# Performance work log

Measured on AMD Instinct MI355X. Metric: run time of the kernel, lower is better.

## Reference

```python
import jax, jax.numpy as jnp
import numpy as np

N, L, S, H, D = 2, 4096, 4096, 8, 32


def setup_inputs() -> dict:
    key = jax.random.key(0)
    kq, kk, kv, km = jax.random.split(key, 4)
    queries = jax.random.normal(kq, (N, L, H, D), dtype=jnp.float32)
    keys = jax.random.normal(kk, (N, S, H, D), dtype=jnp.float32)
    values = jax.random.normal(kv, (N, S, H, D), dtype=jnp.float32)
    q_mask = jnp.ones((N, L), dtype=bool)
    kv_mask = jax.random.randint(km, (N, S), 0, 2).astype(bool)
    return {"queries": queries, "keys": keys, "values": values,
            "q_mask": q_mask, "kv_mask": kv_mask}


def reference(queries, keys, values, q_mask, kv_mask):
    # QK: [N, L, S, H] -- contraction over head dim D (GEMM form of the
    # original broadcast-multiply-sum).
    QK = jnp.einsum('nlhd,nshd->nlsh', queries, keys)
    mask = q_mask[:, :, None] & kv_mask[:, None, :]            # [N, L, S]
    QK = jnp.where(mask[..., None], QK, -jnp.inf)
    softmax_temp = 1.0 / np.sqrt(D).astype(np.float32)
    A = jax.nn.softmax(softmax_temp * QK, axis=2)              # softmax over S
    # weighted value sum: [N, L, H, D]
    return jnp.einsum('nlsh,nshd->nlhd', A, values)
```

## Files before the change

### kernel.cpp

```cpp
#include <hip/hip_runtime.h>
#include <stdint.h>
#include <math.h>


typedef __bf16 bf16x8 __attribute__((ext_vector_type(8)));
typedef float  f32x16 __attribute__((ext_vector_type(16)));
typedef float  f32x4  __attribute__((ext_vector_type(4)));

#define C2 0.25502407414058425f

#define BUF_OFF_B 64

__global__ __launch_bounds__(256) void prep(
    const float* __restrict__ K, const float* __restrict__ V,
    const int* __restrict__ KM, int* __restrict__ W, __bf16* __restrict__ BUF)
{
    const int wib = threadIdx.x >> 6, lane = threadIdx.x & 63;
    const int n = blockIdx.x >> 8;
    __shared__ int csum[64];
    __shared__ int idx[4096];

    const int* m = KM + n * 4096;
    for (int c = wib; c < 64; c += 4) {
        unsigned long long bal = __ballot(m[c * 64 + lane] != 0);
        if (lane == 0) csum[c] = __popcll(bal);
    }
    __syncthreads();
    if (wib == 0) {
        int v = csum[lane];
        #pragma unroll
        for (int off = 1; off < 64; off <<= 1) {
            int u = __shfl_up(v, off);
            if (lane >= off) v += u;
        }
        csum[lane] = v;
    }
    __syncthreads();
    const int total = csum[63];
    for (int c = wib; c < 64; c += 4) {
        bool mm = m[c * 64 + lane] != 0;
        unsigned long long bal = __ballot(mm);
        int base = c ? csum[c - 1] : 0;
        int pre = __popcll(bal & ((1ull << lane) - 1ull));
        if (mm) idx[base + pre] = c * 64 + lane;
    }
    const int cnt32 = (total + 31) & ~31;
    for (int j = total + (int)threadIdx.x; j < cnt32; j += 256) idx[j] = 0;
    __syncthreads();

    if (threadIdx.x == 0 && (blockIdx.x & 255) == 0) W[n] = total;

    const int gt = blockIdx.x * 4 + wib;
    const int h = (gt >> 7) & 7, t = gt & 127;
    if (t >= ((total + 31) >> 5)) return;
    const int hi = lane >> 5, lq = lane & 31;
    const float* Kb = K + (size_t)n * 4096 * 256 + h * 32;
    const float* Vb = V + (size_t)n * 4096 * 256 + h * 32;
    __bf16* dst = BUF + (size_t)gt * 2048 + lane * 8;

    const float* krow = Kb + (size_t)idx[t * 32 + lq] * 256 + 8 * hi;
    #pragma unroll
    for (int f = 0; f < 2; ++f) {
        f32x4 a = *(const f32x4*)(krow + 16 * f);
        f32x4 b = *(const f32x4*)(krow + 16 * f + 4);
        bf16x8 o8;
        o8[0] = (__bf16)a[0]; o8[1] = (__bf16)a[1]; o8[2] = (__bf16)a[2]; o8[3] = (__bf16)a[3];
        o8[4] = (__bf16)b[0]; o8[5] = (__bf16)b[1]; o8[6] = (__bf16)b[2]; o8[7] = (__bf16)b[3];
        *(bf16x8*)(dst + f * 512) = o8;
    }
    #pragma unroll
    for (int f = 0; f < 2; ++f) {
        bf16x8 o8;
        #pragma unroll
        for (int j = 0; j < 8; ++j) {
            int s = t * 32 + 16 * f + (j & 3) + 4 * hi + 8 * ((j >> 2) & 1);
            o8[j] = (__bf16)Vb[(size_t)idx[s] * 256 + lq];
        }
        *(bf16x8*)(dst + 1024 + f * 512) = o8;
    }
}

__global__ __launch_bounds__(256, 4) void fattn32(
    const float* __restrict__ Q, const __bf16* __restrict__ BUF,
    const int* __restrict__ W, float* __restrict__ Out)
{
    constexpr int L = 4096, H = 8, D = 32, RS = H * D;
    const int lane = threadIdx.x & 63;
    const int wib  = threadIdx.x >> 6;
    const int w    = (blockIdx.x & 7) * 256 + (blockIdx.x >> 3);
    const int qt   = w & 127;
    const int h    = (w >> 7) & 7;
    const int n    = w >> 10;
    const int hi   = lane >> 5;
    const int lq   = lane & 31;

    const int cnt    = W[n];
    const int ntiles = (cnt + 31) >> 5;

    const float* qrow = Q + ((size_t)n * L + qt * 32 + lq) * RS + h * D + 8 * hi;
    bf16x8 qf0, qf1;
    {
        f32x4 a0 = *(const f32x4*)(qrow);
        f32x4 b0 = *(const f32x4*)(qrow + 4);
        f32x4 a1 = *(const f32x4*)(qrow + 16);
        f32x4 b1 = *(const f32x4*)(qrow + 20);
        #pragma unroll
        for (int j = 0; j < 4; ++j) {
            qf0[j]     = (__bf16)(C2 * a0[j]);
            qf0[4 + j] = (__bf16)(C2 * b0[j]);
            qf1[j]     = (__bf16)(C2 * a1[j]);
            qf1[4 + j] = (__bf16)(C2 * b1[j]);
        }
    }

    const __bf16* bufp = BUF + (size_t)((n * 8 + h) * 128) * 2048 + lane * 8;

    f32x16 o = {};
    float l = 0.0f;
    const f32x16 z = {};

    int t = wib;
    const __bf16* tb = bufp + (size_t)t * 2048;
    bf16x8 ck0 = *(const bf16x8*)(tb);
    bf16x8 ck1 = *(const bf16x8*)(tb + 512);
    bf16x8 cv0 = *(const bf16x8*)(tb + 1024);
    bf16x8 cv1 = *(const bf16x8*)(tb + 1536);

    for (; t < ntiles; t += 4) {
        const int tn = (t + 4 < ntiles) ? t + 4 : t;
        const __bf16* nb = bufp + (size_t)tn * 2048;
        bf16x8 nk0 = *(const bf16x8*)(nb);
        bf16x8 nk1 = *(const bf16x8*)(nb + 512);
        bf16x8 nv0 = *(const bf16x8*)(nb + 1024);
        bf16x8 nv1 = *(const bf16x8*)(nb + 1536);

        f32x16 st = __builtin_amdgcn_mfma_f32_32x32x16_bf16(ck0, qf0, z, 0, 0, 0);
        st = __builtin_amdgcn_mfma_f32_32x32x16_bf16(ck1, qf1, st, 0, 0, 0);

        float p[16];
        #pragma unroll
        for (int r = 0; r < 16; ++r)
            p[r] = __builtin_amdgcn_exp2f(st[r]);

        const int kb = t * 32;
        if (kb + 32 > cnt) {
            #pragma unroll
            for (int r = 0; r < 16; ++r) {
                int ks = kb + (r & 3) + 8 * ((r >> 2) & 1) + 16 * (r >> 3) + 4 * hi;
                if (ks >= cnt) p[r] = 0.0f;
            }
        }

        l += (((p[0] + p[1]) + (p[2] + p[3])) + ((p[4] + p[5]) + (p[6] + p[7])))
           + (((p[8] + p[9]) + (p[10] + p[11])) + ((p[12] + p[13]) + (p[14] + p[15])));

        bf16x8 pf0, pf1;
        #pragma unroll
        for (int j = 0; j < 8; ++j) { pf0[j] = (__bf16)p[j]; pf1[j] = (__bf16)p[8 + j]; }

        o = __builtin_amdgcn_mfma_f32_32x32x16_bf16(cv0, pf0, o, 0, 0, 0);
        o = __builtin_amdgcn_mfma_f32_32x32x16_bf16(cv1, pf1, o, 0, 0, 0);

        ck0 = nk0; ck1 = nk1; cv0 = nv0; cv1 = nv1;
    }

    __shared__ float xt[4][32 * 33];
    __shared__ float Ls[4][32];

    float lt = l + __shfl_xor(l, 32);
    float* tp = xt[wib];
    #pragma unroll
    for (int r = 0; r < 16; ++r) {
        int d = (r & 3) + 8 * (r >> 2) + 4 * hi;
        tp[lq * 33 + d] = o[r];
    }
    if (hi == 0) Ls[wib][lq] = lt;
    __syncthreads();

    const int q  = threadIdx.x >> 3;
    const int dg = (threadIdx.x & 7) * 4;
    float ltot = Ls[0][q] + Ls[1][q] + Ls[2][q] + Ls[3][q];
    float inv = 1.0f / ltot;
    f32x4 acc = {};
    #pragma unroll
    for (int wv = 0; wv < 4; ++wv) {
        #pragma unroll
        for (int jj = 0; jj < 4; ++jj)
            acc[jj] += xt[wv][q * 33 + dg + jj];
    }
    acc[0] *= inv; acc[1] *= inv; acc[2] *= inv; acc[3] *= inv;
    float* orow = Out + (((size_t)(n * L + qt * 32 + q)) * H + h) * D + dg;
    *(f32x4*)orow = acc;
}

extern "C" void kernel_launch(void* const* d_in, const int* in_sizes, int n_in,
                              void* d_out, int out_size, void* d_ws, size_t ws_size,
                              hipStream_t stream) {
    const float* Q = (const float*)d_in[0];
    const float* K = (const float*)d_in[1];
    const float* V = (const float*)d_in[2];
    const int* KM = (const int*)d_in[4];
    float* Out = (float*)d_out;

    int* Wk = (int*)d_ws;
    __bf16* BUF = (__bf16*)((char*)d_ws + BUF_OFF_B);

    hipLaunchKernelGGL(prep,    dim3(512),  dim3(256), 0, stream, K, V, KM, Wk, BUF);
    hipLaunchKernelGGL(fattn32, dim3(2048), dim3(256), 0, stream, Q, BUF, Wk, Out);
}
```

Before: 45.09 us.

## Share K/V tiles across four query tiles per block via LDS double buffering

Each block now handles four query tiles of the same head, one per wave, instead of splitting the key range of a single query tile across waves. The K/V tile is staged cooperatively into LDS with a double buffer and a barrier each iteration, so each tile is fetched from global memory once per block rather than once per wave. This also drops the cross-wave reduction at the end, because each wave normalises and writes its own output. The cost is a barrier per key tile and 4x fewer blocks (512), which reduces parallelism and latency hiding.

```diff
diff --git a/kernel.cpp b/kernel.cpp
--- a/kernel.cpp
+++ b/kernel.cpp
@@ -84,20 +84,22 @@
     const float* __restrict__ Q, const __bf16* __restrict__ BUF,
     const int* __restrict__ W, float* __restrict__ Out)
 {
-    constexpr int L = 4096, H = 8, D = 32, RS = H * D;
-    const int lane = threadIdx.x & 63;
-    const int wib  = threadIdx.x >> 6;
-    const int w    = (blockIdx.x & 7) * 256 + (blockIdx.x >> 3);
-    const int qt   = w & 127;
-    const int h    = (w >> 7) & 7;
-    const int n    = w >> 10;
-    const int hi   = lane >> 5;
-    const int lq   = lane & 31;
+    const int tid  = threadIdx.x;
+    const int lane = tid & 63;
+    const int wib  = tid >> 6;
+    const int b  = blockIdx.x;
+    const int w  = (b & 7) * 64 + (b >> 3);
+    const int qg = w & 31;
+    const int h  = (w >> 5) & 7;
+    const int n  = w >> 8;
+    const int qt = qg * 4 + wib;
+    const int hi = lane >> 5;
+    const int lq = lane & 31;
 
     const int cnt    = W[n];
     const int ntiles = (cnt + 31) >> 5;
 
-    const float* qrow = Q + ((size_t)n * L + qt * 32 + lq) * RS + h * D + 8 * hi;
+    const float* qrow = Q + ((size_t)n * 4096 + qt * 32 + lq) * 256 + h * 32 + 8 * hi;
     bf16x8 qf0, qf1;
     {
         f32x4 a0 = *(const f32x4*)(qrow);
@@ -113,29 +115,32 @@
         }
     }
 
-    const __bf16* bufp = BUF + (size_t)((n * 8 + h) * 128) * 2048 + lane * 8;
+    __shared__ float pool[4352];
+    uint8_t* sb = (uint8_t*)pool;
+
+    const uint8_t* bufbase = (const uint8_t*)BUF + (size_t)((n * 8 + h) * 128) * 4096;
+    const uint8_t* ssrc = bufbase + tid * 16;
 
     f32x16 o = {};
     float l = 0.0f;
     const f32x16 z = {};
 
-    int t = wib;
-    const __bf16* tb = bufp + (size_t)t * 2048;
-    bf16x8 ck0 = *(const bf16x8*)(tb);
-    bf16x8 ck1 = *(const bf16x8*)(tb + 512);
-    bf16x8 cv0 = *(const bf16x8*)(tb + 1024);
-    bf16x8 cv1 = *(const bf16x8*)(tb + 1536);
-
-    for (; t < ntiles; t += 4) {
-        const int tn = (t + 4 < ntiles) ? t + 4 : t;
-        const __bf16* nb = bufp + (size_t)tn * 2048;
-        bf16x8 nk0 = *(const bf16x8*)(nb);
-        bf16x8 nk1 = *(const bf16x8*)(nb + 512);
-        bf16x8 nv0 = *(const bf16x8*)(nb + 1024);
-        bf16x8 nv1 = *(const bf16x8*)(nb + 1536);
-
-        f32x16 st = __builtin_amdgcn_mfma_f32_32x32x16_bf16(ck0, qf0, z, 0, 0, 0);
-        st = __builtin_amdgcn_mfma_f32_32x32x16_bf16(ck1, qf1, st, 0, 0, 0);
+    uint4 stg = *(const uint4*)(ssrc);
+
+    for (int t = 0; t < ntiles; ++t) {
+        *(uint4*)(sb + (t & 1) * 4096 + tid * 16) = stg;
+        if (t + 1 < ntiles)
+            stg = *(const uint4*)(ssrc + (size_t)(t + 1) * 4096);
+        asm volatile("s_waitcnt lgkmcnt(0)\n\ts_barrier" ::: "memory");
+
+        const __bf16* tb = (const __bf16*)(sb + (t & 1) * 4096) + lane * 8;
+        bf16x8 kf0 = *(const bf16x8*)(tb);
+        bf16x8 kf1 = *(const bf16x8*)(tb + 512);
+        bf16x8 vf0 = *(const bf16x8*)(tb + 1024);
+        bf16x8 vf1 = *(const bf16x8*)(tb + 1536);
+
+        f32x16 st = __builtin_amdgcn_mfma_f32_32x32x16_bf16(kf0, qf0, z, 0, 0, 0);
+        st = __builtin_amdgcn_mfma_f32_32x32x16_bf16(kf1, qf1, st, 0, 0, 0);
 
         float p[16];
         #pragma unroll
@@ -158,39 +163,33 @@
         #pragma unroll
         for (int j = 0; j < 8; ++j) { pf0[j] = (__bf16)p[j]; pf1[j] = (__bf16)p[8 + j]; }
 
-        o = __builtin_amdgcn_mfma_f32_32x32x16_bf16(cv0, pf0, o, 0, 0, 0);
-        o = __builtin_amdgcn_mfma_f32_32x32x16_bf16(cv1, pf1, o, 0, 0, 0);
-
-        ck0 = nk0; ck1 = nk1; cv0 = nv0; cv1 = nv1;
-    }
-
-    __shared__ float xt[4][32 * 33];
-    __shared__ float Ls[4][32];
-
-    float lt = l + __shfl_xor(l, 32);
-    float* tp = xt[wib];
+        o = __builtin_amdgcn_mfma_f32_32x32x16_bf16(vf0, pf0, o, 0, 0, 0);
+        o = __builtin_amdgcn_mfma_f32_32x32x16_bf16(vf1, pf1, o, 0, 0, 0);
+    }
+
+    float lt  = l + __shfl_xor(l, 32);
+    float inv = 1.0f / lt;
+    __syncthreads();
+    float* tp = pool + wib * 1056;
     #pragma unroll
     for (int r = 0; r < 16; ++r) {
         int d = (r & 3) + 8 * (r >> 2) + 4 * hi;
-        tp[lq * 33 + d] = o[r];
-    }
-    if (hi == 0) Ls[wib][lq] = lt;
-    __syncthreads();
-
-    const int q  = threadIdx.x >> 3;
-    const int dg = (threadIdx.x & 7) * 4;
-    float ltot = Ls[0][q] + Ls[1][q] + Ls[2][q] + Ls[3][q];
-    float inv = 1.0f / ltot;
-    f32x4 acc = {};
-    #pragma unroll
-    for (int wv = 0; wv < 4; ++wv) {
-        #pragma unroll
-        for (int jj = 0; jj < 4; ++jj)
-            acc[jj] += xt[wv][q * 33 + dg + jj];
-    }
-    acc[0] *= inv; acc[1] *= inv; acc[2] *= inv; acc[3] *= inv;
-    float* orow = Out + (((size_t)(n * L + qt * 32 + q)) * H + h) * D + dg;
-    *(f32x4*)orow = acc;
+        tp[lq * 33 + d] = o[r] * inv;
+    }
+    asm volatile("s_waitcnt lgkmcnt(0)" ::: "memory");
+
+    const int qr = lane >> 1;
+    const int dh = (lane & 1) * 16;
+    float* orow = Out + (((size_t)(n * 4096 + qt * 32 + qr)) * 8 + h) * 32 + dh;
+    #pragma unroll
+    for (int k2 = 0; k2 < 4; ++k2) {
+        f32x4 vst;
+        vst[0] = tp[qr * 33 + dh + 4 * k2 + 0];
+        vst[1] = tp[qr * 33 + dh + 4 * k2 + 1];
+        vst[2] = tp[qr * 33 + dh + 4 * k2 + 2];
+        vst[3] = tp[qr * 33 + dh + 4 * k2 + 3];
+        *(f32x4*)(orow + 4 * k2) = vst;
+    }
 }
 
 extern "C" void kernel_launch(void* const* d_in, const int* in_sizes, int n_in,
@@ -205,6 +204,6 @@
     int* Wk = (int*)d_ws;
     __bf16* BUF = (__bf16*)((char*)d_ws + BUF_OFF_B);
 
-    hipLaunchKernelGGL(prep,    dim3(512),  dim3(256), 0, stream, K, V, KM, Wk, BUF);
-    hipLaunchKernelGGL(fattn32, dim3(2048), dim3(256), 0, stream, Q, BUF, Wk, Out);
+    hipLaunchKernelGGL(prep,    dim3(512), dim3(256), 0, stream, K, V, KM, Wk, BUF);
+    hipLaunchKernelGGL(fattn32, dim3(512), dim3(256), 0, stream, Q, BUF, Wk, Out);
 }
```

After: 46.49 us. 1.03x slower.
